# Performance work log

Measured on AMD Instinct MI355X. Metric: run time of the kernel, lower is better.

Reference implementation:

```python
import jax, jax.numpy as jnp
import numpy as np

# Dims from LiftSplatShootGPN defaults
B, N, D, FH, FW, C = 8, 6, 41, 8, 22, 64
OGFH, OGFW = 128, 352
DX = jnp.array([0.5, 0.5, 20.0], dtype=jnp.float32)        # gen_dx_bx
BX = jnp.array([-49.75, -49.75, 0.0], dtype=jnp.float32)
NX = (200, 200, 1)


def _frustum():
    # D x fH x fW x 3, matches create_frustum
    ds = jnp.broadcast_to(jnp.arange(4.0, 45.0, 1.0, dtype=jnp.float32).reshape(D, 1, 1), (D, FH, FW))
    xs = jnp.broadcast_to(jnp.linspace(0.0, OGFW - 1.0, FW, dtype=jnp.float32).reshape(1, 1, FW), (D, FH, FW))
    ys = jnp.broadcast_to(jnp.linspace(0.0, OGFH - 1.0, FH, dtype=jnp.float32).reshape(1, FH, 1), (D, FH, FW))
    return jnp.stack((xs, ys, ds), -1)


def setup_inputs() -> dict:
    key = jax.random.key(0)
    k1, k2, k3, k4, k5, k6 = jax.random.split(key, 6)
    eye = jnp.eye(3, dtype=jnp.float32)
    x_feats = jax.random.normal(k1, (B, N, D, FH, FW, C), dtype=jnp.float32)
    # well-conditioned camera extrinsics / intrinsics
    rots = eye + 0.1 * jax.random.normal(k2, (B, N, 3, 3), dtype=jnp.float32)
    trans = 2.0 * jax.random.normal(k3, (B, N, 3), dtype=jnp.float32)
    intr_base = jnp.array([[278.0, 0.0, 176.0], [0.0, 278.0, 64.0], [0.0, 0.0, 1.0]], dtype=jnp.float32)
    intrins = intr_base + 0.5 * jax.random.normal(k4, (B, N, 3, 3), dtype=jnp.float32) * jnp.array([[1, 0, 1], [0, 1, 1], [0, 0, 0]], dtype=jnp.float32)
    post_rots = eye + 0.01 * jax.random.normal(k5, (B, N, 3, 3), dtype=jnp.float32)
    post_trans = 0.5 * jax.random.normal(k6, (B, N, 3), dtype=jnp.float32)
    return {"x_feats": x_feats, "rots": rots, "trans": trans, "intrins": intrins,
            "post_rots": post_rots, "post_trans": post_trans}


def _forward(x_feats, rots, trans, intrins, post_rots, post_trans):
    frustum = _frustum()  # [D,FH,FW,3]
    # get_geometry: undo image-space augmentation
    pts = frustum[None, None] - post_trans[:, :, None, None, None, :]            # [B,N,D,H,W,3]
    inv_pr = jnp.linalg.inv(post_rots)                                           # [B,N,3,3]
    pts = jnp.einsum('bnij,bndhwj->bndhwi', inv_pr, pts)
    # unproject: (u*d, v*d, d)
    pts = jnp.concatenate((pts[..., :2] * pts[..., 2:3], pts[..., 2:3]), axis=-1)
    combine = jnp.einsum('bnij,bnjk->bnik', rots, jnp.linalg.inv(intrins))
    geom = jnp.einsum('bnij,bndhwj->bndhwi', combine, pts) + trans[:, :, None, None, None, :]

    # voxel_pooling
    Nprime = B * N * D * FH * FW
    x = x_feats.reshape(Nprime, C)
    # torch .long() truncates toward zero -> astype(int32) matches
    g = ((geom - (BX - DX / 2.0)) / DX).reshape(Nprime, 3).astype(jnp.int32)
    bix = jnp.repeat(jnp.arange(B, dtype=jnp.int32), Nprime // B)
    kept = ((g[:, 0] >= 0) & (g[:, 0] < NX[0]) &
            (g[:, 1] >= 0) & (g[:, 1] < NX[1]) &
            (g[:, 2] >= 0) & (g[:, 2] < NX[2]))
    # QuickCumsum computes per-voxel segment sums; scatter-add of all kept points
    # into the dense grid yields identical values without the sort.
    flat = ((bix * NX[2] + g[:, 2]) * NX[0] + g[:, 0]) * NX[1] + g[:, 1]
    flat = jnp.where(kept, flat, 0)
    xm = jnp.where(kept[:, None], x, jnp.zeros((), x.dtype))
    grid = jnp.zeros((B * NX[2] * NX[0] * NX[1], C), dtype=x.dtype).at[flat].add(xm)
    # final: [B, C, nz, nx0, nx1] -> cat over nz (nz=1) -> [B, C, 200, 200]
    grid = grid.reshape(B, NX[2], NX[0], NX[1], C)
    final = jnp.transpose(grid, (0, 1, 4, 2, 3)).reshape(B, NX[2] * C, NX[0], NX[1])
    return final


def reference(x_feats, rots, trans, intrins, post_rots, post_trans):
    return _forward(x_feats, rots, trans, intrins, post_rots, post_trans)
```

## Files before the change

kernel.cpp:

```cpp
#include <hip/hip_runtime.h>

#define B_   8
#define N_   6
#define D_   41
#define FH_  8
#define FW_  22
#define C_   64
#define NPRIME (B_*N_*D_*FH_*FW_)
#define NBLK_PTS 1353
#define NX0  200
#define NX1  200
#define G1Q  4
#define NB2  (B_ * NX0 * G1Q)
#define OUTSZ (B_*C_*NX0*NX1)
#define CAP  128
#define DIRECT_N 16
#define MAXTASKS 16384
#define GATHER_BLOCKS 1024

__device__ void lapack_inv3_f32(const float Ain[9], float Aout[9]) {
    #pragma clang fp contract(off)
    float a[9];
    for (int r = 0; r < 3; ++r)
        for (int c = 0; c < 3; ++c)
            a[c*3 + r] = Ain[r*3 + c];
    int ipiv[3];
    for (int j = 0; j < 3; ++j) {
        int p = j;
        float amax = fabsf(a[j*3 + j]);
        for (int i = j + 1; i < 3; ++i) {
            float v = fabsf(a[j*3 + i]);
            if (v > amax) { amax = v; p = i; }
        }
        ipiv[j] = p;
        if (p != j)
            for (int c = 0; c < 3; ++c) { float t = a[c*3+j]; a[c*3+j] = a[c*3+p]; a[c*3+p] = t; }
        float d = 1.0f / a[j*3 + j];
        for (int i = j + 1; i < 3; ++i) a[j*3 + i] = a[j*3 + i] * d;
        for (int jj = j + 1; jj < 3; ++jj) {
            float temp = -a[jj*3 + j];
            for (int ii = j + 1; ii < 3; ++ii)
                a[jj*3 + ii] = a[jj*3 + ii] + a[j*3 + ii] * temp;
        }
    }
    for (int j = 0; j < 3; ++j) {
        float ajj_inv = 1.0f / a[j*3 + j];
        a[j*3 + j] = ajj_inv;
        float AJJ = -ajj_inv;
        for (int jj = 0; jj < j; ++jj) {
            float temp = a[j*3 + jj];
            for (int i = 0; i < jj; ++i)
                a[j*3 + i] = a[j*3 + i] + temp * a[jj*3 + i];
            a[j*3 + jj] = a[j*3 + jj] * a[jj*3 + jj];
        }
        for (int i = 0; i < j; ++i) a[j*3 + i] = a[j*3 + i] * AJJ;
    }
    float work[3];
    for (int j = 2; j >= 0; --j) {
        for (int i = j + 1; i < 3; ++i) { work[i] = a[j*3 + i]; a[j*3 + i] = 0.0f; }
        for (int jj = j + 1; jj < 3; ++jj) {
            float temp = -work[jj];
            for (int i = 0; i < 3; ++i)
                a[j*3 + i] = a[j*3 + i] + temp * a[jj*3 + i];
        }
    }
    for (int j = 2; j >= 0; --j) {
        int p = ipiv[j];
        if (p != j)
            for (int i = 0; i < 3; ++i) { float t = a[j*3+i]; a[j*3+i] = a[p*3+i]; a[p*3+i] = t; }
    }
    for (int r = 0; r < 3; ++r)
        for (int c = 0; c < 3; ++c)
            Aout[r*3 + c] = a[c*3 + r];
}

__global__ void prep_kernel(const float* __restrict__ rots,
                            const float* __restrict__ trans,
                            const float* __restrict__ intrins,
                            const float* __restrict__ post_rots,
                            const float* __restrict__ post_trans,
                            float* __restrict__ mats,
                            int* __restrict__ counts) {
    #pragma clang fp contract(off)
    int t = threadIdx.x;
    for (int i = t; i < NB2; i += 256) counts[i] = 0;
    if (t >= B_ * N_) return;
    float pr[9], ipr[9], K[9], iK[9];
    for (int i = 0; i < 9; ++i) { pr[i] = post_rots[t*9 + i]; K[i] = intrins[t*9 + i]; }
    lapack_inv3_f32(pr, ipr);
    lapack_inv3_f32(K, iK);
    float* m = mats + t * 24;
    for (int i = 0; i < 9; ++i) m[i] = ipr[i];
    for (int i = 0; i < 3; ++i)
        for (int k = 0; k < 3; ++k) {
            float s = rots[t*9 + i*3 + 0] * iK[0*3 + k];
            s = s + rots[t*9 + i*3 + 1] * iK[1*3 + k];
            s = s + rots[t*9 + i*3 + 2] * iK[2*3 + k];
            m[9 + i*3 + k] = s;
        }
    for (int i = 0; i < 3; ++i) {
        m[18 + i] = post_trans[t*3 + i];
        m[21 + i] = trans[t*3 + i];
    }
}

__global__ void __launch_bounds__(256) geom_kernel(
        const float* __restrict__ mats,
        unsigned int* __restrict__ pcode,
        int* __restrict__ counts,
        float4* __restrict__ out4) {
    #pragma clang fp contract(off)
    __shared__ unsigned int hist[NB2];
    int t = threadIdx.x;
    int p = blockIdx.x * 256 + t;
    for (int i = t; i < NB2; i += 256) hist[i] = 0u;
    __syncthreads();

    int w  = p % FW_;
    int h  = (p / FW_) % FH_;
    int d  = (p / (FW_ * FH_)) % D_;
    int bn = p / (FW_ * FH_ * D_);
    int b  = bn / N_;

    const float* m = mats + bn * 24;

    float xs = (w == FW_ - 1) ? 351.0f : (float)((double)w * (351.0 / 21.0));
    float ys = (h == FH_ - 1) ? 127.0f : (float)((double)h * (127.0 / 7.0));
    float ds = 4.0f + (float)d;

    float px = xs - m[18], py = ys - m[19], pz = ds - m[20];
    float qx = m[0]*px;  qx = qx + m[1]*py;  qx = qx + m[2]*pz;
    float qy = m[3]*px;  qy = qy + m[4]*py;  qy = qy + m[5]*pz;
    float qz = m[6]*px;  qz = qz + m[7]*py;  qz = qz + m[8]*pz;

    float ux = qx * qz, uy = qy * qz, uz = qz;

    float gx = m[9]*ux;   gx = gx + m[10]*uy;  gx = gx + m[11]*uz;  gx = gx + m[21];
    float gy = m[12]*ux;  gy = gy + m[13]*uy;  gy = gy + m[14]*uz;  gy = gy + m[22];
    float gz = m[15]*ux;  gz = gz + m[16]*uy;  gz = gz + m[17]*uz;  gz = gz + m[23];

    float cx = (gx - (-50.0f)) / 0.5f;
    float cy = (gy - (-50.0f)) / 0.5f;
    float cz = (gz - (-10.0f)) / 20.0f;
    int g0 = (int)cx;
    int g1 = (int)cy;
    int g2 = (int)cz;

    bool kept = (g0 >= 0) && (g0 < NX0) && (g1 >= 0) && (g1 < NX1) && (g2 == 0);
    if (kept) {
        int g1q = g1 / 50;
        int g1r = g1 - g1q * 50;
        int bk  = (b * NX0 + g0) * G1Q + g1q;
        pcode[p] = ((unsigned int)bk << 6) | (unsigned int)g1r;
        atomicAdd(&hist[bk], 1u);
    } else {
        pcode[p] = 0xFFFFFFFFu;
    }
    __syncthreads();
    for (int i = t; i < NB2; i += 256) {
        unsigned int hv = hist[i];
        if (hv) atomicAdd(&counts[i], (int)hv);
    }

    const int TOT4 = OUTSZ / 4;
    float4 z4 = make_float4(0.f, 0.f, 0.f, 0.f);
    for (int i = p; i < TOT4; i += NPRIME) out4[i] = z4;
}

__global__ void scan_kernel(const int* __restrict__ counts,
                            int* __restrict__ offsets,
                            int* __restrict__ cursor,
                            unsigned int* __restrict__ tasks,
                            int* __restrict__ task_count) {
    __shared__ int ts[256];
    __shared__ int tbase_s[256];
    int t = threadIdx.x;
    const int PER = NB2 / 256;
    int base = t * PER;
    int mysum = 0, mytasks = 0;
    for (int j = 0; j < PER; ++j) {
        int c = counts[base + j];
        mysum += c;
        if (c > 0) mytasks += (c + CAP - 1) / CAP;
    }
    ts[t] = mysum;
    tbase_s[t] = mytasks;
    __syncthreads();
    for (int off = 1; off < 256; off <<= 1) {
        int v  = (t >= off) ? ts[t - off] : 0;
        int tv = (t >= off) ? tbase_s[t - off] : 0;
        __syncthreads();
        ts[t] += v;
        tbase_s[t] += tv;
        __syncthreads();
    }
    int run  = (t > 0) ? ts[t - 1] : 0;
    int tpos = (t > 0) ? tbase_s[t - 1] : 0;
    for (int j = 0; j < PER; ++j) {
        int c = counts[base + j];
        offsets[base + j] = run;
        cursor[base + j]  = run;
        run += c;
        if (c > 0) {
            int nch = (c + CAP - 1) / CAP;
            unsigned int sole = (nch == 1) ? (1u << 31) : 0u;
            for (int k = 0; k < nch; ++k)
                tasks[tpos++] = sole | ((unsigned int)(base + j) << 12) | (unsigned int)k;
        }
    }
    if (t == 255) {
        offsets[NB2] = run;
        task_count[0] = tbase_s[255];
    }
}

__global__ void __launch_bounds__(256) place_kernel(
        const unsigned int* __restrict__ pcode,
        int* __restrict__ cursor,
        unsigned int* __restrict__ entries) {
    __shared__ int cnt[NB2];
    int t = threadIdx.x;
    int p = blockIdx.x * 256 + t;
    for (int i = t; i < NB2; i += 256) cnt[i] = 0;
    __syncthreads();
    unsigned int code = pcode[p];
    bool kept = (code != 0xFFFFFFFFu);
    int bk = (int)(code >> 6);
    int lr = 0;
    if (kept) lr = atomicAdd(&cnt[bk], 1);
    __syncthreads();
    for (int i = t; i < NB2; i += 256) {
        int c = cnt[i];
        if (c) cnt[i] = atomicAdd(&cursor[i], c);
    }
    __syncthreads();
    if (kept)
        entries[cnt[bk] + lr] = ((code & 63u) << 19) | (unsigned int)p;
}

#define LDS_STRIDE 51
__global__ void __launch_bounds__(512) gather_kernel(
        const float* __restrict__ x_feats,
        const unsigned int* __restrict__ entries,
        const int* __restrict__ offsets,
        const unsigned int* __restrict__ tasks,
        const int* __restrict__ task_count,
        float* __restrict__ out) {
    __shared__ float acc[C_ * LDS_STRIDE];
    int ntask = task_count[0];
    int t = threadIdx.x, wave = t >> 6, lane = t & 63;

    for (int tid = blockIdx.x; tid < ntask; tid += GATHER_BLOCKS) {
        unsigned int task = tasks[tid];
        int sole = (int)(task >> 31);
        int bk   = (int)((task >> 12) & 0x1FFFu);
        int ch   = (int)(task & 0xFFFu);
        int s = offsets[bk] + ch * CAP;
        int e = offsets[bk + 1];
        if (e > s + CAP) e = s + CAP;
        int n = e - s;

        int b   = bk / (NX0 * G1Q);
        int rem = bk % (NX0 * G1Q);
        int g0  = rem / G1Q, g1q = rem % G1Q;
        size_t obase = (size_t)b * (C_ * NX0 * NX1) + (size_t)g0 * NX1 + g1q * 50;

        if (n <= DIRECT_N) {
            for (int i = wave; i < n; i += 8) {
                unsigned int v = entries[s + i];
                float f = x_feats[(size_t)(v & 0x7FFFFu) * C_ + lane];
                unsafeAtomicAdd(&out[obase + (size_t)lane * (NX0 * NX1) + (int)(v >> 19)], f);
            }
            continue;
        }

        for (int i = t; i < C_ * LDS_STRIDE; i += 512) acc[i] = 0.0f;
        __syncthreads();

        int nfull = (n >> 6) << 6;
        for (int sbase = 0; sbase < nfull; sbase += 64) {
            int i0 = s + sbase + wave * 8;
            unsigned int v0 = entries[i0],     v1 = entries[i0 + 1];
            unsigned int v2 = entries[i0 + 2], v3 = entries[i0 + 3];
            unsigned int v4 = entries[i0 + 4], v5 = entries[i0 + 5];
            unsigned int v6 = entries[i0 + 6], v7 = entries[i0 + 7];
            float f0 = x_feats[(size_t)(v0 & 0x7FFFFu) * C_ + lane];
            float f1 = x_feats[(size_t)(v1 & 0x7FFFFu) * C_ + lane];
            float f2 = x_feats[(size_t)(v2 & 0x7FFFFu) * C_ + lane];
            float f3 = x_feats[(size_t)(v3 & 0x7FFFFu) * C_ + lane];
            float f4 = x_feats[(size_t)(v4 & 0x7FFFFu) * C_ + lane];
            float f5 = x_feats[(size_t)(v5 & 0x7FFFFu) * C_ + lane];
            float f6 = x_feats[(size_t)(v6 & 0x7FFFFu) * C_ + lane];
            float f7 = x_feats[(size_t)(v7 & 0x7FFFFu) * C_ + lane];
            int lb = lane * LDS_STRIDE;
            atomicAdd(&acc[lb + (int)(v0 >> 19)], f0);
            atomicAdd(&acc[lb + (int)(v1 >> 19)], f1);
            atomicAdd(&acc[lb + (int)(v2 >> 19)], f2);
            atomicAdd(&acc[lb + (int)(v3 >> 19)], f3);
            atomicAdd(&acc[lb + (int)(v4 >> 19)], f4);
            atomicAdd(&acc[lb + (int)(v5 >> 19)], f5);
            atomicAdd(&acc[lb + (int)(v6 >> 19)], f6);
            atomicAdd(&acc[lb + (int)(v7 >> 19)], f7);
        }
        for (int i = nfull + wave; i < n; i += 8) {
            unsigned int v = entries[s + i];
            float f = x_feats[(size_t)(v & 0x7FFFFu) * C_ + lane];
            atomicAdd(&acc[lane * LDS_STRIDE + (int)(v >> 19)], f);
        }
        __syncthreads();

        for (int k = t; k < C_ * 50; k += 512) {
            int c = k / 50, r = k - c * 50;
            float val = acc[c * LDS_STRIDE + r];
            if (val != 0.0f) {
                float* dst = &out[obase + (size_t)c * (NX0 * NX1) + r];
                if (sole) *dst = val;
                else unsafeAtomicAdd(dst, val);
            }
        }
        __syncthreads();
    }
}

extern "C" void kernel_launch(void* const* d_in, const int* in_sizes, int n_in,
                              void* d_out, int out_size, void* d_ws, size_t ws_size,
                              hipStream_t stream) {
    const float* x_feats    = (const float*)d_in[0];
    const float* rots       = (const float*)d_in[1];
    const float* trans      = (const float*)d_in[2];
    const float* intrins    = (const float*)d_in[3];
    const float* post_rots  = (const float*)d_in[4];
    const float* post_trans = (const float*)d_in[5];
    float* out = (float*)d_out;

    char* w = (char*)d_ws;
    float*        mats       = (float*)w;         w += 48 * 24 * sizeof(float);
    int*          counts     = (int*)w;           w += NB2 * sizeof(int);
    int*          offsets    = (int*)w;           w += (NB2 + 1) * sizeof(int);
    int*          cursor     = (int*)w;           w += NB2 * sizeof(int);
    int*          task_count = (int*)w;           w += 4 * sizeof(int);
    unsigned int* tasks      = (unsigned int*)w;  w += MAXTASKS * sizeof(unsigned int);
    unsigned int* pcode      = (unsigned int*)w;  w += NPRIME * sizeof(unsigned int);
    unsigned int* entries    = (unsigned int*)w;  w += NPRIME * sizeof(unsigned int);

    prep_kernel<<<1, 256, 0, stream>>>(rots, trans, intrins, post_rots, post_trans,
                                       mats, counts);
    geom_kernel<<<NBLK_PTS, 256, 0, stream>>>(mats, pcode, counts, (float4*)out);
    scan_kernel<<<1, 256, 0, stream>>>(counts, offsets, cursor, tasks, task_count);
    place_kernel<<<NBLK_PTS, 256, 0, stream>>>(pcode, cursor, entries);
    gather_kernel<<<GATHER_BLOCKS, 512, 0, stream>>>(x_feats, entries, offsets,
                                                     tasks, task_count, out);
}
```

Measured before the change: 207.0 us.

## Give each bucket one gather task, sorted by size, and write output directly

Removes the separate zero-fill of the output in geom_kernel. The gather kernel now owns every output bucket: empty buckets are zero-filled with float2 stores, and non-empty buckets are accumulated in LDS and written with plain vectorized stores instead of atomics. The scan kernel no longer splits buckets into CAP-sized chunks. It classifies buckets into heavy, medium, light and empty classes and orders the task list heaviest first for load balance. The risk is that very large buckets can no longer be split across blocks, which may lengthen the tail.

```diff
diff --git a/kernel.cpp b/kernel.cpp
--- a/kernel.cpp
+++ b/kernel.cpp
@@ -13,10 +13,10 @@
 #define G1Q  4
 #define NB2  (B_ * NX0 * G1Q)
 #define OUTSZ (B_*C_*NX0*NX1)
-#define CAP  128
-#define DIRECT_N 16
 #define MAXTASKS 16384
 #define GATHER_BLOCKS 1024
+#define CLS0 384
+#define CLS1 96
 
 __device__ void lapack_inv3_f32(const float Ain[9], float Aout[9]) {
     #pragma clang fp contract(off)
@@ -107,8 +107,7 @@
 __global__ void __launch_bounds__(256) geom_kernel(
         const float* __restrict__ mats,
         unsigned int* __restrict__ pcode,
-        int* __restrict__ counts,
-        float4* __restrict__ out4) {
+        int* __restrict__ counts) {
     #pragma clang fp contract(off)
     __shared__ unsigned int hist[NB2];
     int t = threadIdx.x;
@@ -161,10 +160,6 @@
         unsigned int hv = hist[i];
         if (hv) atomicAdd(&counts[i], (int)hv);
     }
-
-    const int TOT4 = OUTSZ / 4;
-    float4 z4 = make_float4(0.f, 0.f, 0.f, 0.f);
-    for (int i = p; i < TOT4; i += NPRIME) out4[i] = z4;
 }
 
 __global__ void scan_kernel(const int* __restrict__ counts,
@@ -173,44 +168,52 @@
                             unsigned int* __restrict__ tasks,
                             int* __restrict__ task_count) {
     __shared__ int ts[256];
-    __shared__ int tbase_s[256];
+    __shared__ int s0[256], s1[256], s2[256], s3[256];
     int t = threadIdx.x;
     const int PER = NB2 / 256;
     int base = t * PER;
-    int mysum = 0, mytasks = 0;
+    int mysum = 0;
+    int c0 = 0, c1 = 0, c2 = 0, c3 = 0;
     for (int j = 0; j < PER; ++j) {
         int c = counts[base + j];
         mysum += c;
-        if (c > 0) mytasks += (c + CAP - 1) / CAP;
-    }
-    ts[t] = mysum;
-    tbase_s[t] = mytasks;
+        if (c >= CLS0) c0++;
+        else if (c >= CLS1) c1++;
+        else if (c > 0) c2++;
+        else c3++;
+    }
+    ts[t] = mysum; s0[t] = c0; s1[t] = c1; s2[t] = c2; s3[t] = c3;
     __syncthreads();
     for (int off = 1; off < 256; off <<= 1) {
         int v  = (t >= off) ? ts[t - off] : 0;
-        int tv = (t >= off) ? tbase_s[t - off] : 0;
-        __syncthreads();
-        ts[t] += v;
-        tbase_s[t] += tv;
-        __syncthreads();
-    }
-    int run  = (t > 0) ? ts[t - 1] : 0;
-    int tpos = (t > 0) ? tbase_s[t - 1] : 0;
+        int a0 = (t >= off) ? s0[t - off] : 0;
+        int a1 = (t >= off) ? s1[t - off] : 0;
+        int a2 = (t >= off) ? s2[t - off] : 0;
+        int a3 = (t >= off) ? s3[t - off] : 0;
+        __syncthreads();
+        ts[t] += v; s0[t] += a0; s1[t] += a1; s2[t] += a2; s3[t] += a3;
+        __syncthreads();
+    }
+    int run = (t > 0) ? ts[t - 1] : 0;
+    int tot0 = s0[255], tot1 = s1[255], tot2 = s2[255];
+    int p0 = ((t > 0) ? s0[t - 1] : 0);
+    int p1 = tot0 + ((t > 0) ? s1[t - 1] : 0);
+    int p2 = tot0 + tot1 + ((t > 0) ? s2[t - 1] : 0);
+    int p3 = tot0 + tot1 + tot2 + ((t > 0) ? s3[t - 1] : 0);
     for (int j = 0; j < PER; ++j) {
         int c = counts[base + j];
         offsets[base + j] = run;
         cursor[base + j]  = run;
         run += c;
-        if (c > 0) {
-            int nch = (c + CAP - 1) / CAP;
-            unsigned int sole = (nch == 1) ? (1u << 31) : 0u;
-            for (int k = 0; k < nch; ++k)
-                tasks[tpos++] = sole | ((unsigned int)(base + j) << 12) | (unsigned int)k;
-        }
+        unsigned int bkid = (unsigned int)(base + j);
+        if (c >= CLS0)      tasks[p0++] = bkid;
+        else if (c >= CLS1) tasks[p1++] = bkid;
+        else if (c > 0)     tasks[p2++] = bkid;
+        else                tasks[p3++] = bkid;
     }
     if (t == 255) {
         offsets[NB2] = run;
-        task_count[0] = tbase_s[255];
+        task_count[0] = NB2;
     }
 }
 
@@ -244,20 +247,14 @@
         const unsigned int* __restrict__ entries,
         const int* __restrict__ offsets,
         const unsigned int* __restrict__ tasks,
-        const int* __restrict__ task_count,
         float* __restrict__ out) {
     __shared__ float acc[C_ * LDS_STRIDE];
-    int ntask = task_count[0];
     int t = threadIdx.x, wave = t >> 6, lane = t & 63;
 
-    for (int tid = blockIdx.x; tid < ntask; tid += GATHER_BLOCKS) {
-        unsigned int task = tasks[tid];
-        int sole = (int)(task >> 31);
-        int bk   = (int)((task >> 12) & 0x1FFFu);
-        int ch   = (int)(task & 0xFFFu);
-        int s = offsets[bk] + ch * CAP;
+    for (int tid = blockIdx.x; tid < NB2; tid += GATHER_BLOCKS) {
+        int bk = (int)tasks[tid];
+        int s = offsets[bk];
         int e = offsets[bk + 1];
-        if (e > s + CAP) e = s + CAP;
         int n = e - s;
 
         int b   = bk / (NX0 * G1Q);
@@ -265,11 +262,11 @@
         int g0  = rem / G1Q, g1q = rem % G1Q;
         size_t obase = (size_t)b * (C_ * NX0 * NX1) + (size_t)g0 * NX1 + g1q * 50;
 
-        if (n <= DIRECT_N) {
-            for (int i = wave; i < n; i += 8) {
-                unsigned int v = entries[s + i];
-                float f = x_feats[(size_t)(v & 0x7FFFFu) * C_ + lane];
-                unsafeAtomicAdd(&out[obase + (size_t)lane * (NX0 * NX1) + (int)(v >> 19)], f);
+        if (n == 0) {
+            float2 z2 = make_float2(0.f, 0.f);
+            for (int k = t; k < C_ * 25; k += 512) {
+                int c = k / 25, r2 = k - c * 25;
+                *(float2*)&out[obase + (size_t)c * (NX0 * NX1) + (size_t)(r2 * 2)] = z2;
             }
             continue;
         }
@@ -309,14 +306,11 @@
         }
         __syncthreads();
 
-        for (int k = t; k < C_ * 50; k += 512) {
-            int c = k / 50, r = k - c * 50;
-            float val = acc[c * LDS_STRIDE + r];
-            if (val != 0.0f) {
-                float* dst = &out[obase + (size_t)c * (NX0 * NX1) + r];
-                if (sole) *dst = val;
-                else unsafeAtomicAdd(dst, val);
-            }
+        for (int k = t; k < C_ * 25; k += 512) {
+            int c = k / 25, r2 = k - c * 25;
+            float2 v = make_float2(acc[c * LDS_STRIDE + 2 * r2],
+                                   acc[c * LDS_STRIDE + 2 * r2 + 1]);
+            *(float2*)&out[obase + (size_t)c * (NX0 * NX1) + (size_t)(r2 * 2)] = v;
         }
         __syncthreads();
     }
@@ -345,9 +339,9 @@
 
     prep_kernel<<<1, 256, 0, stream>>>(rots, trans, intrins, post_rots, post_trans,
                                        mats, counts);
-    geom_kernel<<<NBLK_PTS, 256, 0, stream>>>(mats, pcode, counts, (float4*)out);
+    geom_kernel<<<NBLK_PTS, 256, 0, stream>>>(mats, pcode, counts);
     scan_kernel<<<1, 256, 0, stream>>>(counts, offsets, cursor, tasks, task_count);
     place_kernel<<<NBLK_PTS, 256, 0, stream>>>(pcode, cursor, entries);
     gather_kernel<<<GATHER_BLOCKS, 512, 0, stream>>>(x_feats, entries, offsets,
-                                                     tasks, task_count, out);
-}
+                                                     tasks, out);
+}
```

New measurement: 212.9 us. +2.8%, slower.

## Replace dense output zeroing with per-bucket writes and fold prep into geom

Applied to the files above, without the earlier changes.

Removes the separate prep kernel by having each geom block build its camera matrices in shared memory, and replaces it with a memset of the counts. Buckets now cover half a row (100 cells) instead of a quarter, so the output no longer needs a full zeroing pass. Empty and single-chunk buckets write their full slice directly with float4 stores, and only multi-chunk buckets are zeroed in place_kernel before atomic accumulation. Tasks are ordered by size class. This trades extra per-block matrix inversions and larger LDS accumulators for skipping the global zero pass and most global atomics.

```diff
diff --git a/kernel.cpp b/kernel.cpp
--- a/kernel.cpp
+++ b/kernel.cpp
@@ -8,15 +8,17 @@
 #define C_   64
 #define NPRIME (B_*N_*D_*FH_*FW_)
 #define NBLK_PTS 1353
+#define PTS_PER_CAM (D_*FH_*FW_)
 #define NX0  200
 #define NX1  200
-#define G1Q  4
-#define NB2  (B_ * NX0 * G1Q)
+#define G1H  2
+#define NB2  (B_ * NX0 * G1H)
 #define OUTSZ (B_*C_*NX0*NX1)
-#define CAP  128
-#define DIRECT_N 16
 #define MAXTASKS 16384
 #define GATHER_BLOCKS 1024
+#define CAP  384
+#define CLS1 64
+#define LDS_STRIDE 101
 
 __device__ void lapack_inv3_f32(const float Ain[9], float Aout[9]) {
     #pragma clang fp contract(off)
@@ -74,55 +76,61 @@
             Aout[r*3 + c] = a[c*3 + r];
 }
 
-__global__ void prep_kernel(const float* __restrict__ rots,
-                            const float* __restrict__ trans,
-                            const float* __restrict__ intrins,
-                            const float* __restrict__ post_rots,
-                            const float* __restrict__ post_trans,
-                            float* __restrict__ mats,
-                            int* __restrict__ counts) {
+__device__ void build_mats(int bn,
+                           const float* __restrict__ rots,
+                           const float* __restrict__ trans,
+                           const float* __restrict__ intrins,
+                           const float* __restrict__ post_rots,
+                           const float* __restrict__ post_trans,
+                           float* m) {
     #pragma clang fp contract(off)
-    int t = threadIdx.x;
-    for (int i = t; i < NB2; i += 256) counts[i] = 0;
-    if (t >= B_ * N_) return;
     float pr[9], ipr[9], K[9], iK[9];
-    for (int i = 0; i < 9; ++i) { pr[i] = post_rots[t*9 + i]; K[i] = intrins[t*9 + i]; }
+    for (int i = 0; i < 9; ++i) { pr[i] = post_rots[bn*9 + i]; K[i] = intrins[bn*9 + i]; }
     lapack_inv3_f32(pr, ipr);
     lapack_inv3_f32(K, iK);
-    float* m = mats + t * 24;
     for (int i = 0; i < 9; ++i) m[i] = ipr[i];
     for (int i = 0; i < 3; ++i)
         for (int k = 0; k < 3; ++k) {
-            float s = rots[t*9 + i*3 + 0] * iK[0*3 + k];
-            s = s + rots[t*9 + i*3 + 1] * iK[1*3 + k];
-            s = s + rots[t*9 + i*3 + 2] * iK[2*3 + k];
+            float s = rots[bn*9 + i*3 + 0] * iK[0*3 + k];
+            s = s + rots[bn*9 + i*3 + 1] * iK[1*3 + k];
+            s = s + rots[bn*9 + i*3 + 2] * iK[2*3 + k];
             m[9 + i*3 + k] = s;
         }
     for (int i = 0; i < 3; ++i) {
-        m[18 + i] = post_trans[t*3 + i];
-        m[21 + i] = trans[t*3 + i];
+        m[18 + i] = post_trans[bn*3 + i];
+        m[21 + i] = trans[bn*3 + i];
     }
 }
 
 __global__ void __launch_bounds__(256) geom_kernel(
-        const float* __restrict__ mats,
+        const float* __restrict__ rots,
+        const float* __restrict__ trans,
+        const float* __restrict__ intrins,
+        const float* __restrict__ post_rots,
+        const float* __restrict__ post_trans,
         unsigned int* __restrict__ pcode,
-        int* __restrict__ counts,
-        float4* __restrict__ out4) {
+        int* __restrict__ counts) {
     #pragma clang fp contract(off)
     __shared__ unsigned int hist[NB2];
+    __shared__ float smats[2][24];
     int t = threadIdx.x;
     int p = blockIdx.x * 256 + t;
+    int p0blk = blockIdx.x * 256;
+    int bnA = p0blk / PTS_PER_CAM;
+    int bnB = (p0blk + 255) / PTS_PER_CAM;
     for (int i = t; i < NB2; i += 256) hist[i] = 0u;
+    if (t == 0)  build_mats(bnA, rots, trans, intrins, post_rots, post_trans, smats[0]);
+    if (t == 64 && bnB != bnA)
+                 build_mats(bnB, rots, trans, intrins, post_rots, post_trans, smats[1]);
     __syncthreads();
 
     int w  = p % FW_;
     int h  = (p / FW_) % FH_;
     int d  = (p / (FW_ * FH_)) % D_;
-    int bn = p / (FW_ * FH_ * D_);
+    int bn = p / PTS_PER_CAM;
     int b  = bn / N_;
 
-    const float* m = mats + bn * 24;
+    const float* m = smats[bn - bnA];
 
     float xs = (w == FW_ - 1) ? 351.0f : (float)((double)w * (351.0 / 21.0));
     float ys = (h == FH_ - 1) ? 127.0f : (float)((double)h * (127.0 / 7.0));
@@ -148,10 +156,10 @@
 
     bool kept = (g0 >= 0) && (g0 < NX0) && (g1 >= 0) && (g1 < NX1) && (g2 == 0);
     if (kept) {
-        int g1q = g1 / 50;
-        int g1r = g1 - g1q * 50;
-        int bk  = (b * NX0 + g0) * G1Q + g1q;
-        pcode[p] = ((unsigned int)bk << 6) | (unsigned int)g1r;
+        int g1h = g1 / 100;
+        int r   = g1 - g1h * 100;
+        int bk  = (b * NX0 + g0) * G1H + g1h;
+        pcode[p] = ((unsigned int)bk << 7) | (unsigned int)r;
         atomicAdd(&hist[bk], 1u);
     } else {
         pcode[p] = 0xFFFFFFFFu;
@@ -161,63 +169,76 @@
         unsigned int hv = hist[i];
         if (hv) atomicAdd(&counts[i], (int)hv);
     }
-
-    const int TOT4 = OUTSZ / 4;
-    float4 z4 = make_float4(0.f, 0.f, 0.f, 0.f);
-    for (int i = p; i < TOT4; i += NPRIME) out4[i] = z4;
 }
 
 __global__ void scan_kernel(const int* __restrict__ counts,
                             int* __restrict__ offsets,
                             int* __restrict__ cursor,
                             unsigned int* __restrict__ tasks,
-                            int* __restrict__ task_count) {
-    __shared__ int ts[256];
-    __shared__ int tbase_s[256];
+                            int* __restrict__ task_count,
+                            int* __restrict__ zlist) {
+    __shared__ int ts[128], s0[128], s1[128], s2[128], s3[128], s4[128];
     int t = threadIdx.x;
-    const int PER = NB2 / 256;
+    const int PER = NB2 / 128;
     int base = t * PER;
-    int mysum = 0, mytasks = 0;
+    int mysum = 0, c0 = 0, c1 = 0, c2 = 0, c3 = 0, c4 = 0;
     for (int j = 0; j < PER; ++j) {
         int c = counts[base + j];
         mysum += c;
-        if (c > 0) mytasks += (c + CAP - 1) / CAP;
-    }
-    ts[t] = mysum;
-    tbase_s[t] = mytasks;
-    __syncthreads();
-    for (int off = 1; off < 256; off <<= 1) {
+        if (c > CAP)       { c0 += (c + CAP - 1) / CAP; c4++; }
+        else if (c >= CLS1) c1++;
+        else if (c > 0)     c2++;
+        else                c3++;
+    }
+    ts[t] = mysum; s0[t] = c0; s1[t] = c1; s2[t] = c2; s3[t] = c3; s4[t] = c4;
+    __syncthreads();
+    for (int off = 1; off < 128; off <<= 1) {
         int v  = (t >= off) ? ts[t - off] : 0;
-        int tv = (t >= off) ? tbase_s[t - off] : 0;
-        __syncthreads();
-        ts[t] += v;
-        tbase_s[t] += tv;
+        int a0 = (t >= off) ? s0[t - off] : 0;
+        int a1 = (t >= off) ? s1[t - off] : 0;
+        int a2 = (t >= off) ? s2[t - off] : 0;
+        int a3 = (t >= off) ? s3[t - off] : 0;
+        int a4 = (t >= off) ? s4[t - off] : 0;
+        __syncthreads();
+        ts[t] += v; s0[t] += a0; s1[t] += a1; s2[t] += a2; s3[t] += a3; s4[t] += a4;
         __syncthreads();
     }
     int run  = (t > 0) ? ts[t - 1] : 0;
-    int tpos = (t > 0) ? tbase_s[t - 1] : 0;
+    int tot0 = s0[127], tot1 = s1[127], tot2 = s2[127], tot3 = s3[127];
+    int p0 = ((t > 0) ? s0[t - 1] : 0);
+    int p1 = tot0 + ((t > 0) ? s1[t - 1] : 0);
+    int p2 = tot0 + tot1 + ((t > 0) ? s2[t - 1] : 0);
+    int p3 = tot0 + tot1 + tot2 + ((t > 0) ? s3[t - 1] : 0);
+    int pz = ((t > 0) ? s4[t - 1] : 0);
     for (int j = 0; j < PER; ++j) {
-        int c = counts[base + j];
-        offsets[base + j] = run;
-        cursor[base + j]  = run;
+        int bk = base + j;
+        int c = counts[bk];
+        offsets[bk] = run;
+        cursor[bk]  = run;
         run += c;
-        if (c > 0) {
+        if (c > CAP) {
             int nch = (c + CAP - 1) / CAP;
-            unsigned int sole = (nch == 1) ? (1u << 31) : 0u;
             for (int k = 0; k < nch; ++k)
-                tasks[tpos++] = sole | ((unsigned int)(base + j) << 12) | (unsigned int)k;
-        }
-    }
-    if (t == 255) {
+                tasks[p0++] = ((unsigned int)bk << 12) | (unsigned int)k;
+            zlist[pz++] = bk;
+        } else if (c >= CLS1) tasks[p1++] = (1u << 31) | ((unsigned int)bk << 12);
+        else if (c > 0)       tasks[p2++] = (1u << 31) | ((unsigned int)bk << 12);
+        else                  tasks[p3++] = (1u << 31) | ((unsigned int)bk << 12);
+    }
+    if (t == 127) {
         offsets[NB2] = run;
-        task_count[0] = tbase_s[255];
+        task_count[0] = tot0 + tot1 + tot2 + tot3;
+        task_count[1] = s4[127];
     }
 }
 
 __global__ void __launch_bounds__(256) place_kernel(
         const unsigned int* __restrict__ pcode,
         int* __restrict__ cursor,
-        unsigned int* __restrict__ entries) {
+        unsigned int* __restrict__ entries,
+        const int* __restrict__ task_count,
+        const int* __restrict__ zlist,
+        float* __restrict__ out) {
     __shared__ int cnt[NB2];
     int t = threadIdx.x;
     int p = blockIdx.x * 256 + t;
@@ -225,7 +246,7 @@
     __syncthreads();
     unsigned int code = pcode[p];
     bool kept = (code != 0xFFFFFFFFu);
-    int bk = (int)(code >> 6);
+    int bk = (int)(code >> 7);
     int lr = 0;
     if (kept) lr = atomicAdd(&cnt[bk], 1);
     __syncthreads();
@@ -235,10 +256,23 @@
     }
     __syncthreads();
     if (kept)
-        entries[cnt[bk] + lr] = ((code & 63u) << 19) | (unsigned int)p;
-}
-
-#define LDS_STRIDE 51
+        entries[cnt[bk] + lr] = ((code & 127u) << 19) | (unsigned int)p;
+
+    int nz = task_count[1];
+    int tot = nz * (C_ * 25);
+    float4 z4 = make_float4(0.f, 0.f, 0.f, 0.f);
+    for (int k = p; k < tot; k += NPRIME) {
+        int zi = k / (C_ * 25), rem = k - zi * (C_ * 25);
+        int zbk = zlist[zi];
+        int b = zbk / (NX0 * G1H);
+        int rr = zbk % (NX0 * G1H);
+        int g0 = rr >> 1, g1h = rr & 1;
+        size_t obase = (size_t)b * (C_ * NX0 * NX1) + (size_t)g0 * NX1 + g1h * 100;
+        int c = rem / 25, r4 = rem - c * 25;
+        *(float4*)&out[obase + (size_t)c * (NX0 * NX1) + 4 * r4] = z4;
+    }
+}
+
 __global__ void __launch_bounds__(512) gather_kernel(
         const float* __restrict__ x_feats,
         const unsigned int* __restrict__ entries,
@@ -253,23 +287,23 @@
     for (int tid = blockIdx.x; tid < ntask; tid += GATHER_BLOCKS) {
         unsigned int task = tasks[tid];
         int sole = (int)(task >> 31);
-        int bk   = (int)((task >> 12) & 0x1FFFu);
+        int bk   = (int)((task >> 12) & 0xFFFu);
         int ch   = (int)(task & 0xFFFu);
         int s = offsets[bk] + ch * CAP;
         int e = offsets[bk + 1];
-        if (e > s + CAP) e = s + CAP;
+        if (!sole && e > s + CAP) e = s + CAP;
         int n = e - s;
 
-        int b   = bk / (NX0 * G1Q);
-        int rem = bk % (NX0 * G1Q);
-        int g0  = rem / G1Q, g1q = rem % G1Q;
-        size_t obase = (size_t)b * (C_ * NX0 * NX1) + (size_t)g0 * NX1 + g1q * 50;
-
-        if (n <= DIRECT_N) {
-            for (int i = wave; i < n; i += 8) {
-                unsigned int v = entries[s + i];
-                float f = x_feats[(size_t)(v & 0x7FFFFu) * C_ + lane];
-                unsafeAtomicAdd(&out[obase + (size_t)lane * (NX0 * NX1) + (int)(v >> 19)], f);
+        int b   = bk / (NX0 * G1H);
+        int rem = bk % (NX0 * G1H);
+        int g0  = rem >> 1, g1h = rem & 1;
+        size_t obase = (size_t)b * (C_ * NX0 * NX1) + (size_t)g0 * NX1 + g1h * 100;
+
+        if (n == 0) {
+            float4 z4 = make_float4(0.f, 0.f, 0.f, 0.f);
+            for (int k = t; k < C_ * 25; k += 512) {
+                int c = k / 25, r4 = k - c * 25;
+                *(float4*)&out[obase + (size_t)c * (NX0 * NX1) + 4 * r4] = z4;
             }
             continue;
         }
@@ -309,13 +343,20 @@
         }
         __syncthreads();
 
-        for (int k = t; k < C_ * 50; k += 512) {
-            int c = k / 50, r = k - c * 50;
-            float val = acc[c * LDS_STRIDE + r];
-            if (val != 0.0f) {
-                float* dst = &out[obase + (size_t)c * (NX0 * NX1) + r];
-                if (sole) *dst = val;
-                else unsafeAtomicAdd(dst, val);
+        if (sole) {
+            for (int k = t; k < C_ * 25; k += 512) {
+                int c = k / 25, r4 = k - c * 25;
+                int lbase = c * LDS_STRIDE + 4 * r4;
+                float4 v = make_float4(acc[lbase], acc[lbase + 1],
+                                       acc[lbase + 2], acc[lbase + 3]);
+                *(float4*)&out[obase + (size_t)c * (NX0 * NX1) + 4 * r4] = v;
+            }
+        } else {
+            for (int k = t; k < C_ * 100; k += 512) {
+                int c = k / 100, r = k - c * 100;
+                float val = acc[c * LDS_STRIDE + r];
+                if (val != 0.0f)
+                    unsafeAtomicAdd(&out[obase + (size_t)c * (NX0 * NX1) + r], val);
             }
         }
         __syncthreads();
@@ -334,20 +375,22 @@
     float* out = (float*)d_out;
 
     char* w = (char*)d_ws;
-    float*        mats       = (float*)w;         w += 48 * 24 * sizeof(float);
     int*          counts     = (int*)w;           w += NB2 * sizeof(int);
     int*          offsets    = (int*)w;           w += (NB2 + 1) * sizeof(int);
     int*          cursor     = (int*)w;           w += NB2 * sizeof(int);
     int*          task_count = (int*)w;           w += 4 * sizeof(int);
     unsigned int* tasks      = (unsigned int*)w;  w += MAXTASKS * sizeof(unsigned int);
+    int*          zlist      = (int*)w;           w += NB2 * sizeof(int);
     unsigned int* pcode      = (unsigned int*)w;  w += NPRIME * sizeof(unsigned int);
     unsigned int* entries    = (unsigned int*)w;  w += NPRIME * sizeof(unsigned int);
 
-    prep_kernel<<<1, 256, 0, stream>>>(rots, trans, intrins, post_rots, post_trans,
-                                       mats, counts);
-    geom_kernel<<<NBLK_PTS, 256, 0, stream>>>(mats, pcode, counts, (float4*)out);
-    scan_kernel<<<1, 256, 0, stream>>>(counts, offsets, cursor, tasks, task_count);
-    place_kernel<<<NBLK_PTS, 256, 0, stream>>>(pcode, cursor, entries);
+    hipMemsetAsync(counts, 0, NB2 * sizeof(int), stream);
+    geom_kernel<<<NBLK_PTS, 256, 0, stream>>>(rots, trans, intrins, post_rots,
+                                              post_trans, pcode, counts);
+    scan_kernel<<<1, 128, 0, stream>>>(counts, offsets, cursor, tasks,
+                                       task_count, zlist);
+    place_kernel<<<NBLK_PTS, 256, 0, stream>>>(pcode, cursor, entries,
+                                               task_count, zlist, out);
     gather_kernel<<<GATHER_BLOCKS, 512, 0, stream>>>(x_feats, entries, offsets,
                                                      tasks, task_count, out);
 }
```

New measurement: 210.7 us. Within noise of the previous version (+1.7%).
